# Kernel optimization log

Measured on AMD Instinct MI355X. Metric: run time of the kernel, lower is better.

Reference implementation:

```python
import jax, jax.numpy as jnp
import numpy as np
from jax import lax

BETA = 0.95
THRESH = 1.0
NUM_INPUTS, NUM_HIDDEN, NUM_CLASSES, NUM_STEPS, BATCH = 80, 256, 2, 200, 4096


@jax.custom_vjp
def spike_fn(x):
    # Heaviside spike; surrogate gradient = fast_sigmoid (slope=25)
    return (x > 0).astype(x.dtype)

def _spike_fwd(x):
    return spike_fn(x), x

def _spike_bwd(x, g):
    slope = 25.0
    return (g / (slope * jnp.abs(x) + 1.0) ** 2,)

spike_fn.defvjp(_spike_fwd, _spike_bwd)


def _linear_init(key, fan_in, fan_out):
    # torch nn.Linear default init: U(-1/sqrt(fan_in), 1/sqrt(fan_in))
    k1, k2 = jax.random.split(key)
    bound = 1.0 / np.sqrt(fan_in)
    W = jax.random.uniform(k1, (fan_out, fan_in), jnp.float32, -bound, bound)
    b = jax.random.uniform(k2, (fan_out,), jnp.float32, -bound, bound)
    return W, b


def setup_inputs() -> dict:
    key = jax.random.key(0)
    kx, k1, k2, k3, k4 = jax.random.split(key, 5)
    x = jax.random.normal(kx, (BATCH, NUM_INPUTS, NUM_STEPS), jnp.float32)
    W1, b1 = _linear_init(k1, NUM_INPUTS, NUM_HIDDEN)
    W2, b2 = _linear_init(k2, NUM_HIDDEN, NUM_HIDDEN)
    W3, b3 = _linear_init(k3, NUM_HIDDEN, NUM_HIDDEN)
    W4, b4 = _linear_init(k4, NUM_HIDDEN, NUM_CLASSES)
    return {"x": x, "W1": W1, "b1": b1, "W2": W2, "b2": b2,
            "W3": W3, "b3": b3, "W4": W4, "b4": b4}


def _lif(cur, mem):
    # snntorch Leaky, reset_mechanism='subtract': reset from previous mem (detached)
    reset = lax.stop_gradient((mem > THRESH).astype(mem.dtype))
    mem = BETA * mem + cur - reset * THRESH
    spk = spike_fn(mem - THRESH)
    return spk, mem


def reference(x, W1, b1, W2, b2, W3, b3, W4, b4):
    B = x.shape[0]
    xt = jnp.transpose(x, (2, 0, 1))  # [T, B, 80]
    m1 = jnp.zeros((B, NUM_HIDDEN), x.dtype)
    m2 = jnp.zeros((B, NUM_HIDDEN), x.dtype)
    m3 = jnp.zeros((B, NUM_HIDDEN), x.dtype)
    m4 = jnp.zeros((B, NUM_CLASSES), x.dtype)

    def step(carry, x_t):
        m1, m2, m3, m4 = carry
        s1, m1 = _lif(x_t @ W1.T + b1, m1)
        s2, m2 = _lif(s1 @ W2.T + b2, m2)
        s3, m3 = _lif(s2 @ W3.T + b3, m3)
        s4, m4 = _lif(s3 @ W4.T + b4, m4)
        return (m1, m2, m3, m4), s4

    _, spk4_rec = lax.scan(step, (m1, m2, m3, m4), xt)
    return spk4_rec  # [T, B, num_classes]
```

## Files before the change

kernel.cpp:

```cpp
#include <hip/hip_runtime.h>
#include <cstddef>


#define BATCH 4096
#define TSTEPS 200
#define NIN 80
#define KP 96
#define NH 256
#define XPAD 104
#define SPAD 264
#define WP1 104

#define W1HI 0
#define W1LO 24576
#define W2HI 49152
#define W2LO 114688
#define W3HI 180224
#define W3LO 245760

#define LO_SCALE 2048.0f
#define LO_INV 4.8828125e-4f

typedef _Float16 h8 __attribute__((ext_vector_type(8)));
typedef float f4 __attribute__((ext_vector_type(4)));

__device__ __forceinline__ void lds_barrier() {
  __builtin_amdgcn_s_waitcnt(0xC07F);
  __builtin_amdgcn_s_barrier();
}

__global__ __launch_bounds__(256) void prep_kernel(
    const float* __restrict__ W1, const float* __restrict__ W2,
    const float* __restrict__ W3, _Float16* __restrict__ ws) {
  unsigned id = blockIdx.x * 256u + threadIdx.x;
  if (id >= 24576u + 65536u + 65536u) return;
  float v;
  unsigned off;
  _Float16 *hi, *lo;
  if (id < 24576u) {
    unsigned n = id / KP, k = id % KP;
    v = (k < NIN) ? W1[n * NIN + k] : 0.0f;
    hi = ws + W1HI; lo = ws + W1LO; off = id;
  } else if (id < 90112u) {
    off = id - 24576u; v = W2[off];
    hi = ws + W2HI; lo = ws + W2LO;
  } else {
    off = id - 90112u; v = W3[off];
    hi = ws + W3HI; lo = ws + W3LO;
  }
  _Float16 h = (_Float16)v;
  float r = (v - (float)h) * LO_SCALE;
  hi[off] = h;
  lo[off] = (_Float16)r;
}

__global__ __attribute__((amdgpu_waves_per_eu(4, 4)))
__launch_bounds__(1024) void snn_kernel(
    const float* __restrict__ x,
    const float* __restrict__ b1, const float* __restrict__ b2,
    const float* __restrict__ b3, const float* __restrict__ W4,
    const float* __restrict__ b4, const _Float16* __restrict__ ws,
    float* __restrict__ out) {
  __shared__ alignas(16) _Float16 Wh1[256][WP1];
  __shared__ alignas(16) _Float16 xAhi[8][16][XPAD];
  __shared__ alignas(16) _Float16 xAlo[8][16][XPAD];
  __shared__ alignas(16) _Float16 S1[16][SPAD];
  __shared__ alignas(16) _Float16 S2[16][SPAD];
  __shared__ alignas(16) _Float16 S3[16][SPAD];

  const int tid = threadIdx.x;
  const int wave = tid >> 6;
  const int lane = tid & 63;
  const int n16 = lane & 15;
  const int kg = lane >> 4;
  const int wb = blockIdx.x << 4;
  const int nn = (wave << 4) + n16;

  for (int c = tid; c < 3072; c += 1024) {
    int row = c / 12, w = c % 12;
    *(h8*)&Wh1[row][w * 8] = *(const h8*)(ws + W1HI + row * KP + w * 8);
  }

  const _Float16* w1l = ws + W1LO + nn * KP;
  const _Float16* w2h = ws + W2HI + nn * NH;
  const _Float16* w2l = ws + W2LO + nn * NH;
  const _Float16* w3h = ws + W3HI + nn * NH;
  const _Float16* w3l = ws + W3LO + nn * NH;

  const float bb1 = b1[nn], bb2 = b2[nn], bb3 = b3[nn];

  const int j4 = lane >> 5;
  const int ks4 = (lane & 31) << 3;
  const float* w4p = W4 + j4 * NH + ks4;
  const float bb4 = b4[j4];

  float mem1[4] = {0.f, 0.f, 0.f, 0.f};
  float mem2[4] = {0.f, 0.f, 0.f, 0.f};
  float mem3[4] = {0.f, 0.f, 0.f, 0.f};
  float mem4 = 0.f;

  for (int t = 0; t < TSTEPS; ++t) {
    const int ph = t & 7;
    if (ph == 0) {
      for (unsigned e = (unsigned)tid; e < 3072u; e += 1024u) {
        unsigned m = e / 192u, r = e % 192u, i = r >> 1, t4 = r & 1u;
        f4 v = {0.f, 0.f, 0.f, 0.f};
        if (i < NIN)
          v = *(const f4*)(x + ((size_t)(wb + m) * NIN + i) * TSTEPS + t +
                           t4 * 4);
#pragma unroll
        for (int s = 0; s < 4; ++s) {
          float f = v[s];
          _Float16 h = (_Float16)f;
          xAhi[t4 * 4 + s][m][i] = h;
          xAlo[t4 * 4 + s][m][i] = (_Float16)((f - (float)h) * LO_SCALE);
        }
      }
      lds_barrier();
    }

    h8 w1lo[3];
#pragma unroll
    for (int kt = 0; kt < 3; ++kt)
      w1lo[kt] = *(const h8*)(w1l + kt * 32 + kg * 8);

    h8 wl2a[4];
#pragma unroll
    for (int q = 0; q < 4; ++q)
      wl2a[q] = *(const h8*)(w2l + q * 32 + kg * 8);

    f4 aH = {0.f, 0.f, 0.f, 0.f};
    f4 aL = {0.f, 0.f, 0.f, 0.f};
#pragma unroll
    for (int kt = 0; kt < 3; ++kt) {
      const int ko = kt * 32 + kg * 8;
      h8 ahi = *(const h8*)&xAhi[ph][n16][ko];
      h8 alo = *(const h8*)&xAlo[ph][n16][ko];
      h8 wh = *(const h8*)&Wh1[nn][ko];
      aH = __builtin_amdgcn_mfma_f32_16x16x32_f16(ahi, wh, aH, 0, 0, 0);
      aL = __builtin_amdgcn_mfma_f32_16x16x32_f16(alo, wh, aL, 0, 0, 0);
      aL = __builtin_amdgcn_mfma_f32_16x16x32_f16(ahi, w1lo[kt], aL, 0, 0, 0);
    }
#pragma unroll
    for (int r = 0; r < 4; ++r) {
      float cur = __fadd_rn(__fadd_rn(aH[r], __fmul_rn(aL[r], LO_INV)), bb1);
      float mo = mem1[r];
      float mn = __fsub_rn(__fadd_rn(__fmul_rn(0.95f, mo), cur),
                           (mo > 1.0f) ? 1.0f : 0.0f);
      mem1[r] = mn;
      S1[kg * 4 + r][nn] = (mn > 1.0f) ? (_Float16)1.0f : (_Float16)0.0f;
    }
    lds_barrier();

    h8 wl2b[4];
#pragma unroll
    for (int q = 0; q < 4; ++q)
      wl2b[q] = *(const h8*)(w2l + (4 + q) * 32 + kg * 8);

    aH = (f4){0.f, 0.f, 0.f, 0.f};
    aL = (f4){0.f, 0.f, 0.f, 0.f};
#pragma unroll
    for (int kt = 0; kt < 8; ++kt) {
      h8 w = *(const h8*)(w2h + kt * 32 + kg * 8);
      h8 a = *(const h8*)&S1[n16][kt * 32 + kg * 8];
      aH = __builtin_amdgcn_mfma_f32_16x16x32_f16(a, w, aH, 0, 0, 0);
    }
#pragma unroll
    for (int q = 0; q < 4; ++q) {
      h8 a = *(const h8*)&S1[n16][q * 32 + kg * 8];
      aL = __builtin_amdgcn_mfma_f32_16x16x32_f16(a, wl2a[q], aL, 0, 0, 0);
    }
    h8 wl3a[4];
#pragma unroll
    for (int q = 0; q < 4; ++q)
      wl3a[q] = *(const h8*)(w3l + q * 32 + kg * 8);
#pragma unroll
    for (int q = 0; q < 4; ++q) {
      h8 a = *(const h8*)&S1[n16][(4 + q) * 32 + kg * 8];
      aL = __builtin_amdgcn_mfma_f32_16x16x32_f16(a, wl2b[q], aL, 0, 0, 0);
    }
#pragma unroll
    for (int r = 0; r < 4; ++r) {
      float cur = __fadd_rn(__fadd_rn(aH[r], __fmul_rn(aL[r], LO_INV)), bb2);
      float mo = mem2[r];
      float mn = __fsub_rn(__fadd_rn(__fmul_rn(0.95f, mo), cur),
                           (mo > 1.0f) ? 1.0f : 0.0f);
      mem2[r] = mn;
      S2[kg * 4 + r][nn] = (mn > 1.0f) ? (_Float16)1.0f : (_Float16)0.0f;
    }
    lds_barrier();

    h8 wl3b[4];
#pragma unroll
    for (int q = 0; q < 4; ++q)
      wl3b[q] = *(const h8*)(w3l + (4 + q) * 32 + kg * 8);

    aH = (f4){0.f, 0.f, 0.f, 0.f};
    aL = (f4){0.f, 0.f, 0.f, 0.f};
#pragma unroll
    for (int kt = 0; kt < 8; ++kt) {
      h8 w = *(const h8*)(w3h + kt * 32 + kg * 8);
      h8 a = *(const h8*)&S2[n16][kt * 32 + kg * 8];
      aH = __builtin_amdgcn_mfma_f32_16x16x32_f16(a, w, aH, 0, 0, 0);
    }
#pragma unroll
    for (int q = 0; q < 4; ++q) {
      h8 a = *(const h8*)&S2[n16][q * 32 + kg * 8];
      aL = __builtin_amdgcn_mfma_f32_16x16x32_f16(a, wl3a[q], aL, 0, 0, 0);
    }
    f4 w4a = *(const f4*)(w4p);
    f4 w4b = *(const f4*)(w4p + 4);
#pragma unroll
    for (int q = 0; q < 4; ++q) {
      h8 a = *(const h8*)&S2[n16][(4 + q) * 32 + kg * 8];
      aL = __builtin_amdgcn_mfma_f32_16x16x32_f16(a, wl3b[q], aL, 0, 0, 0);
    }
#pragma unroll
    for (int r = 0; r < 4; ++r) {
      float cur = __fadd_rn(__fadd_rn(aH[r], __fmul_rn(aL[r], LO_INV)), bb3);
      float mo = mem3[r];
      float mn = __fsub_rn(__fadd_rn(__fmul_rn(0.95f, mo), cur),
                           (mo > 1.0f) ? 1.0f : 0.0f);
      mem3[r] = mn;
      S3[kg * 4 + r][nn] = (mn > 1.0f) ? (_Float16)1.0f : (_Float16)0.0f;
    }
    lds_barrier();

    {
      h8 s = *(const h8*)&S3[wave][ks4];
      float p = 0.0f;
#pragma unroll
      for (int u = 0; u < 4; ++u)
        p = __fadd_rn(p, __fmul_rn((float)s[u], w4a[u]));
#pragma unroll
      for (int u = 0; u < 4; ++u)
        p = __fadd_rn(p, __fmul_rn((float)s[4 + u], w4b[u]));
#pragma unroll
      for (int msk = 1; msk <= 16; msk <<= 1)
        p = __fadd_rn(p, __shfl_xor(p, msk));
      float cur = __fadd_rn(p, bb4);
      float mo = mem4;
      float mn = __fsub_rn(__fadd_rn(__fmul_rn(0.95f, mo), cur),
                           (mo > 1.0f) ? 1.0f : 0.0f);
      mem4 = mn;
      if ((lane & 31) == 0)
        out[(size_t)t * (BATCH * 2) + (size_t)(wb + wave) * 2 + j4] =
            (mn > 1.0f) ? 1.0f : 0.0f;
    }
  }
}

extern "C" void kernel_launch(void* const* d_in, const int* in_sizes, int n_in,
                              void* d_out, int out_size, void* d_ws,
                              size_t ws_size, hipStream_t stream) {
  const float* x  = (const float*)d_in[0];
  const float* W1 = (const float*)d_in[1];
  const float* b1 = (const float*)d_in[2];
  const float* W2 = (const float*)d_in[3];
  const float* b2 = (const float*)d_in[4];
  const float* W3 = (const float*)d_in[5];
  const float* b3 = (const float*)d_in[6];
  const float* W4 = (const float*)d_in[7];
  const float* b4 = (const float*)d_in[8];
  float* out = (float*)d_out;
  _Float16* ws = (_Float16*)d_ws;

  hipLaunchKernelGGL(prep_kernel, dim3(608), dim3(256), 0, stream,
                     W1, W2, W3, ws);
  hipLaunchKernelGGL(snn_kernel, dim3(BATCH / 16), dim3(1024), 0, stream,
                     x, b1, b2, b3, W4, b4, ws, out);
}
```

Before: 2.715 ms.

## Software-pipeline the four SNN layers across timesteps with double-buffered spikes

Restructures the time loop into a skewed wavefront: in iteration p, layer 1 runs timestep p, layer 2 runs p-1, layer 3 runs p-2 and layer 4 runs p-3. Spike buffers S1-S3 are double-buffered, so each iteration needs one barrier instead of four. The aim is to cut barrier stalls and let the independent layer work interleave within a wave. In exchange it adds three warm-up and drain iterations, predicate branches, and more LDS and register pressure from keeping several weight fragments live at once.

```diff
diff --git a/kernel.cpp b/kernel.cpp
--- a/kernel.cpp
+++ b/kernel.cpp
@@ -64,9 +64,9 @@
   __shared__ alignas(16) _Float16 Wh1[256][WP1];
   __shared__ alignas(16) _Float16 xAhi[8][16][XPAD];
   __shared__ alignas(16) _Float16 xAlo[8][16][XPAD];
-  __shared__ alignas(16) _Float16 S1[16][SPAD];
-  __shared__ alignas(16) _Float16 S2[16][SPAD];
-  __shared__ alignas(16) _Float16 S3[16][SPAD];
+  __shared__ alignas(16) _Float16 S1[2][16][SPAD];
+  __shared__ alignas(16) _Float16 S2[2][16][SPAD];
+  __shared__ alignas(16) _Float16 S3[2][16][SPAD];
 
   const int tid = threadIdx.x;
   const int wave = tid >> 6;
@@ -99,14 +99,19 @@
   float mem3[4] = {0.f, 0.f, 0.f, 0.f};
   float mem4 = 0.f;
 
-  for (int t = 0; t < TSTEPS; ++t) {
-    const int ph = t & 7;
-    if (ph == 0) {
+  for (int p = 0; p < TSTEPS + 3; ++p) {
+    const int cur = p & 1;
+    const bool a1 = (p < TSTEPS);
+    const bool a2 = (p >= 1) && (p < TSTEPS + 1);
+    const bool a3 = (p >= 2) && (p < TSTEPS + 2);
+    const bool a4 = (p >= 3) && (p < TSTEPS + 3);
+
+    if (a1 && (p & 7) == 0) {
       for (unsigned e = (unsigned)tid; e < 3072u; e += 1024u) {
         unsigned m = e / 192u, r = e % 192u, i = r >> 1, t4 = r & 1u;
         f4 v = {0.f, 0.f, 0.f, 0.f};
         if (i < NIN)
-          v = *(const f4*)(x + ((size_t)(wb + m) * NIN + i) * TSTEPS + t +
+          v = *(const f4*)(x + ((size_t)(wb + m) * NIN + i) * TSTEPS + p +
                            t4 * 4);
 #pragma unroll
         for (int s = 0; s < 4; ++s) {
@@ -120,133 +125,143 @@
     }
 
     h8 w1lo[3];
-#pragma unroll
-    for (int kt = 0; kt < 3; ++kt)
-      w1lo[kt] = *(const h8*)(w1l + kt * 32 + kg * 8);
-
-    h8 wl2a[4];
-#pragma unroll
-    for (int q = 0; q < 4; ++q)
-      wl2a[q] = *(const h8*)(w2l + q * 32 + kg * 8);
-
-    f4 aH = {0.f, 0.f, 0.f, 0.f};
-    f4 aL = {0.f, 0.f, 0.f, 0.f};
-#pragma unroll
-    for (int kt = 0; kt < 3; ++kt) {
-      const int ko = kt * 32 + kg * 8;
-      h8 ahi = *(const h8*)&xAhi[ph][n16][ko];
-      h8 alo = *(const h8*)&xAlo[ph][n16][ko];
-      h8 wh = *(const h8*)&Wh1[nn][ko];
-      aH = __builtin_amdgcn_mfma_f32_16x16x32_f16(ahi, wh, aH, 0, 0, 0);
-      aL = __builtin_amdgcn_mfma_f32_16x16x32_f16(alo, wh, aL, 0, 0, 0);
-      aL = __builtin_amdgcn_mfma_f32_16x16x32_f16(ahi, w1lo[kt], aL, 0, 0, 0);
-    }
-#pragma unroll
-    for (int r = 0; r < 4; ++r) {
-      float cur = __fadd_rn(__fadd_rn(aH[r], __fmul_rn(aL[r], LO_INV)), bb1);
-      float mo = mem1[r];
-      float mn = __fsub_rn(__fadd_rn(__fmul_rn(0.95f, mo), cur),
-                           (mo > 1.0f) ? 1.0f : 0.0f);
-      mem1[r] = mn;
-      S1[kg * 4 + r][nn] = (mn > 1.0f) ? (_Float16)1.0f : (_Float16)0.0f;
-    }
-    lds_barrier();
-
-    h8 wl2b[4];
-#pragma unroll
-    for (int q = 0; q < 4; ++q)
-      wl2b[q] = *(const h8*)(w2l + (4 + q) * 32 + kg * 8);
-
-    aH = (f4){0.f, 0.f, 0.f, 0.f};
-    aL = (f4){0.f, 0.f, 0.f, 0.f};
-#pragma unroll
-    for (int kt = 0; kt < 8; ++kt) {
-      h8 w = *(const h8*)(w2h + kt * 32 + kg * 8);
-      h8 a = *(const h8*)&S1[n16][kt * 32 + kg * 8];
-      aH = __builtin_amdgcn_mfma_f32_16x16x32_f16(a, w, aH, 0, 0, 0);
-    }
-#pragma unroll
-    for (int q = 0; q < 4; ++q) {
-      h8 a = *(const h8*)&S1[n16][q * 32 + kg * 8];
-      aL = __builtin_amdgcn_mfma_f32_16x16x32_f16(a, wl2a[q], aL, 0, 0, 0);
-    }
-    h8 wl3a[4];
-#pragma unroll
-    for (int q = 0; q < 4; ++q)
-      wl3a[q] = *(const h8*)(w3l + q * 32 + kg * 8);
-#pragma unroll
-    for (int q = 0; q < 4; ++q) {
-      h8 a = *(const h8*)&S1[n16][(4 + q) * 32 + kg * 8];
-      aL = __builtin_amdgcn_mfma_f32_16x16x32_f16(a, wl2b[q], aL, 0, 0, 0);
-    }
-#pragma unroll
-    for (int r = 0; r < 4; ++r) {
-      float cur = __fadd_rn(__fadd_rn(aH[r], __fmul_rn(aL[r], LO_INV)), bb2);
-      float mo = mem2[r];
-      float mn = __fsub_rn(__fadd_rn(__fmul_rn(0.95f, mo), cur),
-                           (mo > 1.0f) ? 1.0f : 0.0f);
-      mem2[r] = mn;
-      S2[kg * 4 + r][nn] = (mn > 1.0f) ? (_Float16)1.0f : (_Float16)0.0f;
-    }
-    lds_barrier();
-
-    h8 wl3b[4];
-#pragma unroll
-    for (int q = 0; q < 4; ++q)
-      wl3b[q] = *(const h8*)(w3l + (4 + q) * 32 + kg * 8);
-
-    aH = (f4){0.f, 0.f, 0.f, 0.f};
-    aL = (f4){0.f, 0.f, 0.f, 0.f};
-#pragma unroll
-    for (int kt = 0; kt < 8; ++kt) {
-      h8 w = *(const h8*)(w3h + kt * 32 + kg * 8);
-      h8 a = *(const h8*)&S2[n16][kt * 32 + kg * 8];
-      aH = __builtin_amdgcn_mfma_f32_16x16x32_f16(a, w, aH, 0, 0, 0);
-    }
-#pragma unroll
-    for (int q = 0; q < 4; ++q) {
-      h8 a = *(const h8*)&S2[n16][q * 32 + kg * 8];
-      aL = __builtin_amdgcn_mfma_f32_16x16x32_f16(a, wl3a[q], aL, 0, 0, 0);
-    }
-    f4 w4a = *(const f4*)(w4p);
-    f4 w4b = *(const f4*)(w4p + 4);
-#pragma unroll
-    for (int q = 0; q < 4; ++q) {
-      h8 a = *(const h8*)&S2[n16][(4 + q) * 32 + kg * 8];
-      aL = __builtin_amdgcn_mfma_f32_16x16x32_f16(a, wl3b[q], aL, 0, 0, 0);
-    }
-#pragma unroll
-    for (int r = 0; r < 4; ++r) {
-      float cur = __fadd_rn(__fadd_rn(aH[r], __fmul_rn(aL[r], LO_INV)), bb3);
-      float mo = mem3[r];
-      float mn = __fsub_rn(__fadd_rn(__fmul_rn(0.95f, mo), cur),
-                           (mo > 1.0f) ? 1.0f : 0.0f);
-      mem3[r] = mn;
-      S3[kg * 4 + r][nn] = (mn > 1.0f) ? (_Float16)1.0f : (_Float16)0.0f;
-    }
-    lds_barrier();
-
-    {
-      h8 s = *(const h8*)&S3[wave][ks4];
-      float p = 0.0f;
+    if (a1) {
+#pragma unroll
+      for (int kt = 0; kt < 3; ++kt)
+        w1lo[kt] = *(const h8*)(w1l + kt * 32 + kg * 8);
+    }
+    h8 wl2a[4], wl2b[4];
+    if (a2) {
+#pragma unroll
+      for (int q = 0; q < 4; ++q)
+        wl2a[q] = *(const h8*)(w2l + q * 32 + kg * 8);
+#pragma unroll
+      for (int q = 0; q < 4; ++q)
+        wl2b[q] = *(const h8*)(w2l + (4 + q) * 32 + kg * 8);
+    }
+    h8 wl3a[4], wl3b[4];
+    f4 w4a, w4b;
+    if (a3) {
+#pragma unroll
+      for (int q = 0; q < 4; ++q)
+        wl3a[q] = *(const h8*)(w3l + q * 32 + kg * 8);
+#pragma unroll
+      for (int q = 0; q < 4; ++q)
+        wl3b[q] = *(const h8*)(w3l + (4 + q) * 32 + kg * 8);
+    }
+    if (a4) {
+      w4a = *(const f4*)(w4p);
+      w4b = *(const f4*)(w4p + 4);
+    }
+
+    if (a1) {
+      const int ph = p & 7;
+      f4 aH = {0.f, 0.f, 0.f, 0.f};
+      f4 aL = {0.f, 0.f, 0.f, 0.f};
+#pragma unroll
+      for (int kt = 0; kt < 3; ++kt) {
+        const int ko = kt * 32 + kg * 8;
+        h8 ahi = *(const h8*)&xAhi[ph][n16][ko];
+        h8 alo = *(const h8*)&xAlo[ph][n16][ko];
+        h8 wh = *(const h8*)&Wh1[nn][ko];
+        aH = __builtin_amdgcn_mfma_f32_16x16x32_f16(ahi, wh, aH, 0, 0, 0);
+        aL = __builtin_amdgcn_mfma_f32_16x16x32_f16(alo, wh, aL, 0, 0, 0);
+        aL = __builtin_amdgcn_mfma_f32_16x16x32_f16(ahi, w1lo[kt], aL, 0, 0, 0);
+      }
+#pragma unroll
+      for (int r = 0; r < 4; ++r) {
+        float cur_ = __fadd_rn(__fadd_rn(aH[r], __fmul_rn(aL[r], LO_INV)), bb1);
+        float mo = mem1[r];
+        float mn = __fsub_rn(__fadd_rn(__fmul_rn(0.95f, mo), cur_),
+                             (mo > 1.0f) ? 1.0f : 0.0f);
+        mem1[r] = mn;
+        S1[cur][kg * 4 + r][nn] = (mn > 1.0f) ? (_Float16)1.0f : (_Float16)0.0f;
+      }
+    }
+
+    if (a2) {
+      f4 aH = {0.f, 0.f, 0.f, 0.f};
+      f4 aL = {0.f, 0.f, 0.f, 0.f};
+#pragma unroll
+      for (int kt = 0; kt < 8; ++kt) {
+        h8 w = *(const h8*)(w2h + kt * 32 + kg * 8);
+        h8 a = *(const h8*)&S1[cur ^ 1][n16][kt * 32 + kg * 8];
+        aH = __builtin_amdgcn_mfma_f32_16x16x32_f16(a, w, aH, 0, 0, 0);
+      }
+#pragma unroll
+      for (int q = 0; q < 4; ++q) {
+        h8 a = *(const h8*)&S1[cur ^ 1][n16][q * 32 + kg * 8];
+        aL = __builtin_amdgcn_mfma_f32_16x16x32_f16(a, wl2a[q], aL, 0, 0, 0);
+      }
+#pragma unroll
+      for (int q = 0; q < 4; ++q) {
+        h8 a = *(const h8*)&S1[cur ^ 1][n16][(4 + q) * 32 + kg * 8];
+        aL = __builtin_amdgcn_mfma_f32_16x16x32_f16(a, wl2b[q], aL, 0, 0, 0);
+      }
+#pragma unroll
+      for (int r = 0; r < 4; ++r) {
+        float cur_ = __fadd_rn(__fadd_rn(aH[r], __fmul_rn(aL[r], LO_INV)), bb2);
+        float mo = mem2[r];
+        float mn = __fsub_rn(__fadd_rn(__fmul_rn(0.95f, mo), cur_),
+                             (mo > 1.0f) ? 1.0f : 0.0f);
+        mem2[r] = mn;
+        S2[cur][kg * 4 + r][nn] = (mn > 1.0f) ? (_Float16)1.0f : (_Float16)0.0f;
+      }
+    }
+
+    if (a3) {
+      f4 aH = {0.f, 0.f, 0.f, 0.f};
+      f4 aL = {0.f, 0.f, 0.f, 0.f};
+#pragma unroll
+      for (int kt = 0; kt < 8; ++kt) {
+        h8 w = *(const h8*)(w3h + kt * 32 + kg * 8);
+        h8 a = *(const h8*)&S2[cur ^ 1][n16][kt * 32 + kg * 8];
+        aH = __builtin_amdgcn_mfma_f32_16x16x32_f16(a, w, aH, 0, 0, 0);
+      }
+#pragma unroll
+      for (int q = 0; q < 4; ++q) {
+        h8 a = *(const h8*)&S2[cur ^ 1][n16][q * 32 + kg * 8];
+        aL = __builtin_amdgcn_mfma_f32_16x16x32_f16(a, wl3a[q], aL, 0, 0, 0);
+      }
+#pragma unroll
+      for (int q = 0; q < 4; ++q) {
+        h8 a = *(const h8*)&S2[cur ^ 1][n16][(4 + q) * 32 + kg * 8];
+        aL = __builtin_amdgcn_mfma_f32_16x16x32_f16(a, wl3b[q], aL, 0, 0, 0);
+      }
+#pragma unroll
+      for (int r = 0; r < 4; ++r) {
+        float cur_ = __fadd_rn(__fadd_rn(aH[r], __fmul_rn(aL[r], LO_INV)), bb3);
+        float mo = mem3[r];
+        float mn = __fsub_rn(__fadd_rn(__fmul_rn(0.95f, mo), cur_),
+                             (mo > 1.0f) ? 1.0f : 0.0f);
+        mem3[r] = mn;
+        S3[cur][kg * 4 + r][nn] = (mn > 1.0f) ? (_Float16)1.0f : (_Float16)0.0f;
+      }
+    }
+
+    if (a4) {
+      h8 s = *(const h8*)&S3[cur ^ 1][wave][ks4];
+      float pdot = 0.0f;
 #pragma unroll
       for (int u = 0; u < 4; ++u)
-        p = __fadd_rn(p, __fmul_rn((float)s[u], w4a[u]));
+        pdot = __fadd_rn(pdot, __fmul_rn((float)s[u], w4a[u]));
 #pragma unroll
       for (int u = 0; u < 4; ++u)
-        p = __fadd_rn(p, __fmul_rn((float)s[4 + u], w4b[u]));
+        pdot = __fadd_rn(pdot, __fmul_rn((float)s[4 + u], w4b[u]));
 #pragma unroll
       for (int msk = 1; msk <= 16; msk <<= 1)
-        p = __fadd_rn(p, __shfl_xor(p, msk));
-      float cur = __fadd_rn(p, bb4);
+        pdot = __fadd_rn(pdot, __shfl_xor(pdot, msk));
+      float cur_ = __fadd_rn(pdot, bb4);
       float mo = mem4;
-      float mn = __fsub_rn(__fadd_rn(__fmul_rn(0.95f, mo), cur),
+      float mn = __fsub_rn(__fadd_rn(__fmul_rn(0.95f, mo), cur_),
                            (mo > 1.0f) ? 1.0f : 0.0f);
       mem4 = mn;
       if ((lane & 31) == 0)
-        out[(size_t)t * (BATCH * 2) + (size_t)(wb + wave) * 2 + j4] =
+        out[(size_t)(p - 3) * (BATCH * 2) + (size_t)(wb + wave) * 2 + j4] =
             (mn > 1.0f) ? 1.0f : 0.0f;
     }
+
+    lds_barrier();
   }
 }
 
```

New measurement: 5.054 ms. +86.1%, slower.
